# Performance work log

Hardware: AMD Instinct MI355X
Metric: run time of the kernel (lower is better)

## Reference

```python
import jax, jax.numpy as jnp
import numpy as np

EPSILON_BASE = 0.1
N_ITERS = 10


def setup_inputs() -> dict:
    key = jax.random.key(0)
    k1, k2 = jax.random.split(key)
    N, D = 8192, 512
    embeddings = jax.random.normal(k1, (N, D), dtype=jnp.float32)
    target_noise = jax.random.normal(k2, (N, D), dtype=jnp.float32)
    return {"embeddings": embeddings, "target_noise": target_noise}


def _l2_normalize(x, axis=1, eps=1e-12):
    # matches torch.nn.functional.normalize (divide by max(norm, eps))
    norm = jnp.sqrt(jnp.sum(x * x, axis=axis, keepdims=True))
    return x / jnp.maximum(norm, eps)


def _sinkhorn(x, y):
    n, d = x.shape
    # normalize_embeddings=True path
    x = _l2_normalize(x, axis=1)
    y = _l2_normalize(y, axis=1)
    epsilon = EPSILON_BASE * 2.0
    # squared euclidean cost: C[i,j] = ||x_i - y_j||^2  (cdist p=2, squared)
    sq_x = jnp.sum(x * x, axis=1, keepdims=True)          # (n,1)
    sq_y = jnp.sum(y * y, axis=1, keepdims=True)          # (n,1)
    C = jnp.maximum(sq_x + sq_y.T - 2.0 * (x @ y.T), 0.0)  # (n,n)
    log_K = -C / epsilon

    def body(carry, _):
        log_u, log_v = carry
        log_u = -jax.nn.logsumexp(log_K + log_v[None, :], axis=1)
        log_v = -jax.nn.logsumexp(log_K.T + log_u[None, :], axis=1)
        return (log_u, log_v), None

    init = (jnp.zeros(n, dtype=x.dtype), jnp.zeros(n, dtype=y.dtype))
    (log_u, log_v), _ = jax.lax.scan(body, init, None, length=N_ITERS)

    log_P = log_u[:, None] + log_K + log_v[None, :]
    P = jnp.clip(jnp.exp(log_P), 0.0, 1.0)
    distance = jnp.sum(P * C) / n

    # nan/inf fallback: 1 - mean cosine similarity (x, y already unit norm)
    fallback = 1.0 - jnp.mean(jnp.sum(x * y, axis=1))
    bad = jnp.isnan(distance) | jnp.isinf(distance)
    return jnp.where(bad, fallback, distance)


def reference(embeddings, target_noise):
    if embeddings.ndim == 3:
        embeddings = embeddings.reshape(-1, embeddings.shape[-1])
        target_noise = target_noise.reshape(-1, target_noise.shape[-1])
    return _sinkhorn(embeddings, target_noise)
```

## Files before the change

### kernel.cpp

```cpp
#include <hip/hip_runtime.h>
#include <hip/hip_bf16.h>
#include <hip/hip_fp16.h>
#include <stdint.h>

#define NROW 8192
#define DIM  512
#define LN2   0.6931471805599453f
#define TEN_LOG2E 14.426950408889634f
#define FP4_DEBIAS 1.0201409f

typedef __attribute__((ext_vector_type(8))) short short8;
typedef __attribute__((ext_vector_type(4))) float f32x4;
typedef __attribute__((ext_vector_type(2))) float f32x2;

#define GLL16(gp, lp) __builtin_amdgcn_global_load_lds( \
    (const __attribute__((address_space(1))) void*)(gp), \
    (__attribute__((address_space(3))) void*)(lp), 16, 0, 0)

__device__ __forceinline__ float block_sum256(float v) {
  #pragma unroll
  for (int off = 32; off > 0; off >>= 1) v += __shfl_down(v, off, 64);
  __shared__ float sb[4];
  const int w = threadIdx.x >> 6;
  if ((threadIdx.x & 63) == 0) sb[w] = v;
  __syncthreads();
  return sb[0] + sb[1] + sb[2] + sb[3];
}

__global__ __launch_bounds__(256) void init_kernel(float* __restrict__ colrcp,
                                                   float* __restrict__ diagacc,
                                                   float* __restrict__ distacc) {
  const int g = blockIdx.x * 256 + threadIdx.x;
  colrcp[g] = 1.0f;
  if (g == 0) { diagacc[0] = 0.f; distacc[0] = 0.f; }
}

__global__ __launch_bounds__(256) void normalize_kernel(
    const float* __restrict__ X, const float* __restrict__ Y,
    __hip_bfloat16* __restrict__ Xn, __hip_bfloat16* __restrict__ Yn,
    float* __restrict__ diagacc) {
  const int wave = threadIdx.x >> 6, lane = threadIdx.x & 63;
  float dsum = 0.f;
  #pragma unroll
  for (int rr = 0; rr < 4; rr++) {
    const int row = blockIdx.x * 16 + wave * 4 + rr;
    const float4* xr = (const float4*)(X + (size_t)row * DIM);
    const float4* yr = (const float4*)(Y + (size_t)row * DIM);
    float4 x0 = xr[lane], x1 = xr[lane + 64];
    float4 y0 = yr[lane], y1 = yr[lane + 64];
    float sx = x0.x*x0.x + x0.y*x0.y + x0.z*x0.z + x0.w*x0.w
             + x1.x*x1.x + x1.y*x1.y + x1.z*x1.z + x1.w*x1.w;
    float sy = y0.x*y0.x + y0.y*y0.y + y0.z*y0.z + y0.w*y0.w
             + y1.x*y1.x + y1.y*y1.y + y1.z*y1.z + y1.w*y1.w;
    float sxy = x0.x*y0.x + x0.y*y0.y + x0.z*y0.z + x0.w*y0.w
              + x1.x*y1.x + x1.y*y1.y + x1.z*y1.z + x1.w*y1.w;
    #pragma unroll
    for (int off = 1; off < 64; off <<= 1) {
      sx  += __shfl_xor(sx, off, 64);
      sy  += __shfl_xor(sy, off, 64);
      sxy += __shfl_xor(sxy, off, 64);
    }
    const float rx = 1.0f / fmaxf(sqrtf(sx), 1e-12f);
    const float ry = 1.0f / fmaxf(sqrtf(sy), 1e-12f);
    if (lane == 0) dsum += sxy * rx * ry;
    ushort4 px, py;
    { __hip_bfloat16 b;
      b = __float2bfloat16(x0.x*rx); px.x = *(unsigned short*)&b;
      b = __float2bfloat16(x0.y*rx); px.y = *(unsigned short*)&b;
      b = __float2bfloat16(x0.z*rx); px.z = *(unsigned short*)&b;
      b = __float2bfloat16(x0.w*rx); px.w = *(unsigned short*)&b;
      b = __float2bfloat16(y0.x*ry); py.x = *(unsigned short*)&b;
      b = __float2bfloat16(y0.y*ry); py.y = *(unsigned short*)&b;
      b = __float2bfloat16(y0.z*ry); py.z = *(unsigned short*)&b;
      b = __float2bfloat16(y0.w*ry); py.w = *(unsigned short*)&b;
    }
    ((ushort4*)(Xn + (size_t)row * DIM))[lane] = px;
    ((ushort4*)(Yn + (size_t)row * DIM))[lane] = py;
    { __hip_bfloat16 b;
      b = __float2bfloat16(x1.x*rx); px.x = *(unsigned short*)&b;
      b = __float2bfloat16(x1.y*rx); px.y = *(unsigned short*)&b;
      b = __float2bfloat16(x1.z*rx); px.z = *(unsigned short*)&b;
      b = __float2bfloat16(x1.w*rx); px.w = *(unsigned short*)&b;
      b = __float2bfloat16(y1.x*ry); py.x = *(unsigned short*)&b;
      b = __float2bfloat16(y1.y*ry); py.y = *(unsigned short*)&b;
      b = __float2bfloat16(y1.z*ry); py.z = *(unsigned short*)&b;
      b = __float2bfloat16(y1.w*ry); py.w = *(unsigned short*)&b;
    }
    ((ushort4*)(Xn + (size_t)row * DIM))[lane + 64] = px;
    ((ushort4*)(Yn + (size_t)row * DIM))[lane + 64] = py;
  }
  if (lane == 0) atomicAdd(diagacc, dsum);
}

__global__ __launch_bounds__(256) void gemm_kernel(
    const __hip_bfloat16* __restrict__ A, const __hip_bfloat16* __restrict__ B,
    uint8_t* __restrict__ KT8, uint8_t* __restrict__ K4g, uint8_t* __restrict__ KT4g) {
  __shared__ int4 smem4[2048];
  const int m0 = blockIdx.y * 128;
  const int n0 = blockIdx.x * 128;
  const int t = threadIdx.x;
  const int wave = t >> 6, lane = t & 63;
  const int wm = (wave & 1) * 64, wn = (wave >> 1) * 64;
  const int fr = lane & 15;
  const int fq = lane >> 4;

  f32x4 acc[4][4];
  #pragma unroll
  for (int i = 0; i < 4; i++)
    #pragma unroll
    for (int j = 0; j < 4; j++) acc[i][j] = (f32x4)0.f;

  const int L0 = t, L1 = t + 256;
  const int ar0 = L0 >> 2, ac0 = L0 & 3;
  const int ar1 = L1 >> 2, ac1 = L1 & 3;
  const int4* Ag0 = (const int4*)A + (size_t)(m0 + ar0) * 64 + ac0;
  const int4* Ag1 = (const int4*)A + (size_t)(m0 + ar1) * 64 + ac1;
  const int4* Bg0 = (const int4*)B + (size_t)(n0 + ar0) * 64 + ac0;
  const int4* Bg1 = (const int4*)B + (size_t)(n0 + ar1) * 64 + ac1;

  {
    int4* AsI4 = smem4;
    int4* BsI4 = smem4 + 512;
    GLL16(Ag0, AsI4 + L0);
    GLL16(Ag1, AsI4 + L1);
    GLL16(Bg0, BsI4 + L0);
    GLL16(Bg1, BsI4 + L1);
  }
  __syncthreads();

  #pragma unroll 2
  for (int kt = 0; kt < 16; ++kt) {
    const int cur = kt & 1;
    if (kt < 15) {
      const int kb = (kt + 1) * 4;
      int4* AsN = smem4 + (cur ^ 1) * 1024;
      int4* BsN = AsN + 512;
      GLL16(Ag0 + kb, AsN + L0);
      GLL16(Ag1 + kb, AsN + L1);
      GLL16(Bg0 + kb, BsN + L0);
      GLL16(Bg1 + kb, BsN + L1);
    }
    const short* As = (const short*)(smem4 + cur * 1024);
    const short* Bs = As + 128 * 32;
    short8 af[4], bfr[4];
    #pragma unroll
    for (int i = 0; i < 4; i++) {
      af[i]  = *(const short8*)&As[(wm + i * 16 + fr) * 32 + fq * 8];
      bfr[i] = *(const short8*)&Bs[(wn + i * 16 + fr) * 32 + fq * 8];
    }
    #pragma unroll
    for (int i = 0; i < 4; i++)
      #pragma unroll
      for (int j = 0; j < 4; j++)
        acc[i][j] = __builtin_amdgcn_mfma_f32_16x16x32_bf16(af[i], bfr[j], acc[i][j], 0, 0, 0);
    __syncthreads();
  }
  uint8_t* tileT8 = (uint8_t*)smem4;
  uint8_t* tileK4 = (uint8_t*)smem4 + 16384;
  uint8_t* tileT4 = (uint8_t*)smem4 + 24576;
  #pragma unroll
  for (int i = 0; i < 4; i++) {
    #pragma unroll
    for (int j = 0; j < 4; j++) {
      const int R  = wm + i * 16 + fq * 4;
      const int Cc = wn + j * 16 + fr;
      const float lk0 = fminf(acc[i][j][0], 1.0f) * TEN_LOG2E;
      const float lk1 = fminf(acc[i][j][1], 1.0f) * TEN_LOG2E;
      const float lk2 = fminf(acc[i][j][2], 1.0f) * TEN_LOG2E;
      const float lk3 = fminf(acc[i][j][3], 1.0f) * TEN_LOG2E;
      int pk = 0;
      pk = __builtin_amdgcn_cvt_pk_fp8_f32(exp2f(lk0), exp2f(lk1), pk, false);
      pk = __builtin_amdgcn_cvt_pk_fp8_f32(exp2f(lk2), exp2f(lk3), pk, true);
      const int a = Cc * 128 + R;
      *(int*)(tileT8 + (a ^ (((a >> 7) & 7) << 4))) = pk;
      const uint32_t nb0 = (uint32_t)fminf(fmaxf(rintf(lk0) + 3.f, 0.f), 15.f);
      const uint32_t nb1 = (uint32_t)fminf(fmaxf(rintf(lk1) + 3.f, 0.f), 15.f);
      const uint32_t nb2 = (uint32_t)fminf(fmaxf(rintf(lk2) + 3.f, 0.f), 15.f);
      const uint32_t nb3 = (uint32_t)fminf(fmaxf(rintf(lk3) + 3.f, 0.f), 15.f);
      const uint16_t t4 = (uint16_t)(nb0 | (nb1 << 4) | (nb2 << 8) | (nb3 << 12));
      *(uint16_t*)(tileT4 + Cc * 64 + (R >> 1)) = t4;
      const uint32_t nall = nb0 | (nb1 << 8) | (nb2 << 16) | (nb3 << 24);
      const uint32_t part = (uint32_t)__shfl_xor((int)nall, 1, 64);
      if ((fr & 1) == 0) {
        const uint32_t mg = nall | (part << 4);
        tileK4[(R + 0) * 64 + (Cc >> 1)] = (uint8_t)(mg);
        tileK4[(R + 1) * 64 + (Cc >> 1)] = (uint8_t)(mg >> 8);
        tileK4[(R + 2) * 64 + (Cc >> 1)] = (uint8_t)(mg >> 16);
        tileK4[(R + 3) * 64 + (Cc >> 1)] = (uint8_t)(mg >> 24);
      }
    }
  }
  __syncthreads();
  {
    const int r = t >> 1, h = (t & 1) * 64;
    uint8_t* gp = KT8 + (size_t)(n0 + r) * NROW + m0 + h;
    #pragma unroll
    for (int q = 0; q < 4; q++) {
      const int a = r * 128 + h + q * 16;
      *(int4*)(gp + q * 16) = *(const int4*)(tileT8 + (a ^ (((a >> 7) & 7) << 4)));
    }
  }
  #pragma unroll
  for (int s2 = 0; s2 < 2; s2++) {
    const int idx = t + s2 * 256;
    const int row = idx >> 2, c4 = idx & 3;
    *(int4*)(K4g  + (size_t)(m0 + row) * (NROW / 2) + (n0 >> 1) + c4 * 16) =
        *(const int4*)(tileK4 + idx * 16);
    *(int4*)(KT4g + (size_t)(n0 + row) * (NROW / 2) + (m0 >> 1) + c4 * 16) =
        *(const int4*)(tileT4 + idx * 16);
  }
}

__global__ __launch_bounds__(256) void pass4_kernel(
    const uint8_t* __restrict__ M4, const float* __restrict__ w,
    float* __restrict__ out) {
  __shared__ float4 wl[2048];
  const int t = threadIdx.x;
  const int wave = t >> 6, lane = t & 63;
  const int x8 = lane & 7;
  const int row0 = blockIdx.x * 16 + wave * 4;
  int4 kr[4][4];
  #pragma unroll
  for (int r = 0; r < 4; r++) {
    const int4* Mr = (const int4*)(M4 + (size_t)(row0 + r) * (NROW / 2));
    #pragma unroll
    for (int c = 0; c < 4; c++) kr[r][c] = Mr[c * 64 + lane];
  }
  #pragma unroll
  for (int c = 0; c < 8; c++) {
    const int j = c * 256 + t;
    wl[j ^ ((j >> 3) & 7)] = ((const float4*)w)[j];
  }
  __syncthreads();
  float a0[4] = {0.f, 0.f, 0.f, 0.f}, a1[4] = {0.f, 0.f, 0.f, 0.f};
  #pragma unroll
  for (int c = 0; c < 4; c++) {
    const int base8 = (c * 64 + lane) * 8;
    float4 w4[8];
    #pragma unroll
    for (int ov = 0; ov < 8; ov++) w4[ov] = wl[base8 + (ov ^ x8)];
    #pragma unroll
    for (int r = 0; r < 4; r++) {
      const int* kd = (const int*)&kr[r][c];
      #pragma unroll
      for (int q = 0; q < 4; q++) {
        const uint32_t d = (uint32_t)kd[q];
        #pragma unroll
        for (int e = 0; e < 8; e++) {
          const uint32_t n = (d >> (e * 4)) & 15u;
          const float kv = __uint_as_float((n + 124u) << 23);
          const float4 ww = w4[q * 2 + (e >> 2)];
          const float wv = ((e & 3) == 0) ? ww.x : ((e & 3) == 1) ? ww.y
                         : ((e & 3) == 2) ? ww.z : ww.w;
          if (e < 4) a0[r] += kv * wv; else a1[r] += kv * wv;
        }
      }
    }
  }
  #pragma unroll
  for (int r = 0; r < 4; r++) {
    float acc = a0[r] + a1[r];
    #pragma unroll
    for (int off = 32; off > 0; off >>= 1) acc += __shfl_down(acc, off, 64);
    if (lane == 0) out[row0 + r] = FP4_DEBIAS / acc;
  }
}

__global__ __launch_bounds__(256) void pass_dist_kernel(
    const uint8_t* __restrict__ KT, const float* __restrict__ u,
    float* __restrict__ distacc) {
  __shared__ float4 wl[2048];
  const int t = threadIdx.x;
  const int wave = t >> 6, lane = t & 63;
  const int xh = (lane >> 1) & 3;
  const int row0 = blockIdx.x * 16 + wave * 4;
  int4 ka[8], kb[8];
  const int4* Mr0 = (const int4*)(KT + (size_t)row0 * NROW);
  #pragma unroll
  for (int c = 0; c < 8; c++) ka[c] = Mr0[c * 64 + lane];
  #pragma unroll
  for (int c = 0; c < 8; c++) {
    const int j = c * 256 + t;
    wl[j ^ ((j >> 3) & 3)] = ((const float4*)u)[j];
  }
  __syncthreads();
  float accd = 0.f;
  #pragma unroll
  for (int r = 0; r < 4; r++) {
    if (r < 3) {
      const int4* Mn = (const int4*)(KT + (size_t)(row0 + r + 1) * NROW);
      #pragma unroll
      for (int c = 0; c < 8; c++) { if (r & 1) ka[c] = Mn[c * 64 + lane]; else kb[c] = Mn[c * 64 + lane]; }
    }
    float acc0 = 0.f, acc1 = 0.f;
    #pragma unroll
    for (int c = 0; c < 8; c++) {
      const int b4 = (c * 64 + lane) * 4;
      const int4 kc = (r & 1) ? kb[c] : ka[c];
      const int* kd = (const int*)&kc;
      #pragma unroll
      for (int q = 0; q < 4; q++) {
        float4 ww = wl[b4 + (q ^ xh)];
        f32x2 lo = __builtin_amdgcn_cvt_pk_f32_fp8(kd[q], false);
        f32x2 hi = __builtin_amdgcn_cvt_pk_f32_fp8(kd[q], true);
        acc0 += lo.x * ww.x + lo.y * ww.y;
        acc1 += hi.x * ww.z + hi.y * ww.w;
      }
    }
    float s = acc0 + acc1;
    #pragma unroll
    for (int off = 1; off < 64; off <<= 1) s += __shfl_xor(s, off, 64);
    const float vj = 1.0f / s;
    #pragma unroll
    for (int c = 0; c < 8; c++) {
      const int b4 = (c * 64 + lane) * 4;
      const int4 kc = (r & 1) ? kb[c] : ka[c];
      const int* kd = (const int*)&kc;
      #pragma unroll
      for (int q = 0; q < 4; q++) {
        float4 ww = wl[b4 + (q ^ xh)];
        f32x2 lo = __builtin_amdgcn_cvt_pk_f32_fp8(kd[q], false);
        f32x2 hi = __builtin_amdgcn_cvt_pk_f32_fp8(kd[q], true);
        float kv[4] = {lo.x, lo.y, hi.x, hi.y};
        float uv[4] = {ww.x, ww.y, ww.z, ww.w};
        #pragma unroll
        for (int e = 0; e < 4; e++) {
          float p = fminf(uv[e] * kv[e] * vj, 1.f);
          float cterm = 2.f - 0.2f * LN2 * __log2f(fmaxf(kv[e], 1e-6f));
          accd += p * cterm;
        }
      }
    }
  }
  float tot = block_sum256(accd);
  if (t == 0) atomicAdd(distacc, tot);
}

__global__ void final_kernel(const float* __restrict__ distacc,
                             const float* __restrict__ diagacc,
                             float* __restrict__ out) {
  if (threadIdx.x == 0 && blockIdx.x == 0) {
    float d = distacc[0] * (1.0f / (float)NROW);
    float fb = 1.0f - diagacc[0] * (1.0f / (float)NROW);
    float v = (isnan(d) || isinf(d)) ? fb : d;
    __hip_bfloat16 b = __float2bfloat16(v);
    unsigned short h = *(unsigned short*)&b;
    ((unsigned int*)out)[0] = ((unsigned int)h << 16) | (unsigned int)h;
  }
}

extern "C" void kernel_launch(void* const* d_in, const int* in_sizes, int n_in,
                              void* d_out, int out_size, void* d_ws, size_t ws_size,
                              hipStream_t stream) {
  (void)in_sizes; (void)n_in; (void)out_size; (void)ws_size;
  const float* X = (const float*)d_in[0];
  const float* Y = (const float*)d_in[1];
  float* out = (float*)d_out;

  char* ws = (char*)d_ws;
  size_t off = 0;
  uint8_t* KT8 = (uint8_t*)(ws + off); off += (size_t)NROW * NROW;
  uint8_t* K4  = (uint8_t*)(ws + off); off += (size_t)NROW * NROW / 2;
  uint8_t* KT4 = (uint8_t*)(ws + off); off += (size_t)NROW * NROW / 2;
  __hip_bfloat16* Xn = (__hip_bfloat16*)(ws + off); off += (size_t)NROW * DIM * 2;
  __hip_bfloat16* Yn = (__hip_bfloat16*)(ws + off); off += (size_t)NROW * DIM * 2;
  float* rowrcp  = (float*)(ws + off); off += NROW * 4;
  float* colrcp  = (float*)(ws + off); off += NROW * 4;
  float* diagacc = (float*)(ws + off); off += 256;
  float* distacc = (float*)(ws + off); off += 256;

  init_kernel<<<32, 256, 0, stream>>>(colrcp, diagacc, distacc);
  normalize_kernel<<<512, 256, 0, stream>>>(X, Y, Xn, Yn, diagacc);
  gemm_kernel<<<dim3(64, 64), 256, 0, stream>>>(Xn, Yn, KT8, K4, KT4);
  for (int it = 0; it < 10; ++it) {
    pass4_kernel<<<512, 256, 0, stream>>>(K4,  colrcp, rowrcp);
    if (it < 9)
      pass4_kernel<<<512, 256, 0, stream>>>(KT4, rowrcp, colrcp);
  }
  pass_dist_kernel<<<512, 256, 0, stream>>>(KT8, rowrcp, distacc);
  final_kernel<<<1, 64, 0, stream>>>(distacc, diagacc, out);
}
```

Before: 472.5 us.

## Swizzle FP4 LDS tiles in GEMM epilogue and use one row per wave in pass4

The GEMM epilogue now XOR-swizzles addresses in the tileT4 and tileK4 shared-memory staging buffers to cut LDS bank conflicts on the scattered nibble writes, and the readback applies the matching swizzle. The pass4 matvec kernel now has each wave handle one row instead of four, and its grid grows from 512 to 2048 blocks. That raises parallelism and lowers register pressure, so occupancy should improve. The cost is that every block reloads the full 32KB weight vector into LDS, which is four times as much w traffic per row.

```diff
diff --git a/kernel.cpp b/kernel.cpp
--- a/kernel.cpp
+++ b/kernel.cpp
@@ -178,15 +178,17 @@
       const uint32_t nb2 = (uint32_t)fminf(fmaxf(rintf(lk2) + 3.f, 0.f), 15.f);
       const uint32_t nb3 = (uint32_t)fminf(fmaxf(rintf(lk3) + 3.f, 0.f), 15.f);
       const uint16_t t4 = (uint16_t)(nb0 | (nb1 << 4) | (nb2 << 8) | (nb3 << 12));
-      *(uint16_t*)(tileT4 + Cc * 64 + (R >> 1)) = t4;
+      { const int A4 = Cc * 64 + (R >> 1);
+        *(uint16_t*)(tileT4 + (A4 ^ (((A4 >> 7) & 7) << 4))) = t4; }
       const uint32_t nall = nb0 | (nb1 << 8) | (nb2 << 16) | (nb3 << 24);
       const uint32_t part = (uint32_t)__shfl_xor((int)nall, 1, 64);
       if ((fr & 1) == 0) {
         const uint32_t mg = nall | (part << 4);
-        tileK4[(R + 0) * 64 + (Cc >> 1)] = (uint8_t)(mg);
-        tileK4[(R + 1) * 64 + (Cc >> 1)] = (uint8_t)(mg >> 8);
-        tileK4[(R + 2) * 64 + (Cc >> 1)] = (uint8_t)(mg >> 16);
-        tileK4[(R + 3) * 64 + (Cc >> 1)] = (uint8_t)(mg >> 24);
+        #pragma unroll
+        for (int k = 0; k < 4; k++) {
+          const int A4 = (R + k) * 64 + (Cc >> 1);
+          tileK4[A4 ^ (((A4 >> 8) & 7) << 4)] = (uint8_t)(mg >> (8 * k));
+        }
       }
     }
   }
@@ -204,10 +206,12 @@
   for (int s2 = 0; s2 < 2; s2++) {
     const int idx = t + s2 * 256;
     const int row = idx >> 2, c4 = idx & 3;
+    const int Ak = idx * 16;
+    const int At = idx * 16;
     *(int4*)(K4g  + (size_t)(m0 + row) * (NROW / 2) + (n0 >> 1) + c4 * 16) =
-        *(const int4*)(tileK4 + idx * 16);
+        *(const int4*)(tileK4 + (Ak ^ (((idx >> 4) & 7) << 4)));
     *(int4*)(KT4g + (size_t)(n0 + row) * (NROW / 2) + (m0 >> 1) + c4 * 16) =
-        *(const int4*)(tileT4 + idx * 16);
+        *(const int4*)(tileT4 + (At ^ (((idx >> 3) & 7) << 4)));
   }
 }
 
@@ -218,52 +222,43 @@
   const int t = threadIdx.x;
   const int wave = t >> 6, lane = t & 63;
   const int x8 = lane & 7;
-  const int row0 = blockIdx.x * 16 + wave * 4;
-  int4 kr[4][4];
-  #pragma unroll
-  for (int r = 0; r < 4; r++) {
-    const int4* Mr = (const int4*)(M4 + (size_t)(row0 + r) * (NROW / 2));
-    #pragma unroll
-    for (int c = 0; c < 4; c++) kr[r][c] = Mr[c * 64 + lane];
-  }
+  const int row = blockIdx.x * 4 + wave;
+  const int4* Mr = (const int4*)(M4 + (size_t)row * (NROW / 2));
+  int4 kr[4];
+  #pragma unroll
+  for (int c = 0; c < 4; c++) kr[c] = Mr[c * 64 + lane];
   #pragma unroll
   for (int c = 0; c < 8; c++) {
     const int j = c * 256 + t;
     wl[j ^ ((j >> 3) & 7)] = ((const float4*)w)[j];
   }
   __syncthreads();
-  float a0[4] = {0.f, 0.f, 0.f, 0.f}, a1[4] = {0.f, 0.f, 0.f, 0.f};
+  float a0 = 0.f, a1 = 0.f;
   #pragma unroll
   for (int c = 0; c < 4; c++) {
     const int base8 = (c * 64 + lane) * 8;
     float4 w4[8];
     #pragma unroll
     for (int ov = 0; ov < 8; ov++) w4[ov] = wl[base8 + (ov ^ x8)];
-    #pragma unroll
-    for (int r = 0; r < 4; r++) {
-      const int* kd = (const int*)&kr[r][c];
-      #pragma unroll
-      for (int q = 0; q < 4; q++) {
-        const uint32_t d = (uint32_t)kd[q];
-        #pragma unroll
-        for (int e = 0; e < 8; e++) {
-          const uint32_t n = (d >> (e * 4)) & 15u;
-          const float kv = __uint_as_float((n + 124u) << 23);
-          const float4 ww = w4[q * 2 + (e >> 2)];
-          const float wv = ((e & 3) == 0) ? ww.x : ((e & 3) == 1) ? ww.y
-                         : ((e & 3) == 2) ? ww.z : ww.w;
-          if (e < 4) a0[r] += kv * wv; else a1[r] += kv * wv;
-        }
+    const int* kd = (const int*)&kr[c];
+    #pragma unroll
+    for (int q = 0; q < 4; q++) {
+      const uint32_t d = (uint32_t)kd[q];
+      #pragma unroll
+      for (int e = 0; e < 8; e++) {
+        const uint32_t n = (d >> (e * 4)) & 15u;
+        const float kv = __uint_as_float((n + 124u) << 23);
+        const float4 ww = w4[q * 2 + (e >> 2)];
+        const float wv = ((e & 3) == 0) ? ww.x : ((e & 3) == 1) ? ww.y
+                       : ((e & 3) == 2) ? ww.z : ww.w;
+        if (e < 4) a0 += kv * wv; else a1 += kv * wv;
       }
     }
   }
-  #pragma unroll
-  for (int r = 0; r < 4; r++) {
-    float acc = a0[r] + a1[r];
-    #pragma unroll
-    for (int off = 32; off > 0; off >>= 1) acc += __shfl_down(acc, off, 64);
-    if (lane == 0) out[row0 + r] = FP4_DEBIAS / acc;
-  }
+  float acc = a0 + a1;
+  #pragma unroll
+  for (int off = 32; off > 0; off >>= 1) acc += __shfl_down(acc, off, 64);
+  if (lane == 0) out[row] = FP4_DEBIAS / acc;
 }
 
 __global__ __launch_bounds__(256) void pass_dist_kernel(
@@ -373,9 +368,9 @@
   normalize_kernel<<<512, 256, 0, stream>>>(X, Y, Xn, Yn, diagacc);
   gemm_kernel<<<dim3(64, 64), 256, 0, stream>>>(Xn, Yn, KT8, K4, KT4);
   for (int it = 0; it < 10; ++it) {
-    pass4_kernel<<<512, 256, 0, stream>>>(K4,  colrcp, rowrcp);
+    pass4_kernel<<<2048, 256, 0, stream>>>(K4,  colrcp, rowrcp);
     if (it < 9)
-      pass4_kernel<<<512, 256, 0, stream>>>(KT4, rowrcp, colrcp);
+      pass4_kernel<<<2048, 256, 0, stream>>>(KT4, rowrcp, colrcp);
   }
   pass_dist_kernel<<<512, 256, 0, stream>>>(KT8, rowrcp, distacc);
   final_kernel<<<1, 64, 0, stream>>>(distacc, diagacc, out);
```

Result: faster. 439.1 us, median of 2 (-7.1%).
